# Kernel tuning notes

Measured on AMD Instinct MI355X. Metric: run time of the kernel, lower is better.

## Reference

```python
import jax, jax.numpy as jnp
import numpy as np
import math

N_HEADS = 4
GELU = lambda x: jax.nn.gelu(x, approximate=False)  # torch nn.GELU default = exact erf

def _ln(x, s, b):
    m = jnp.mean(x, axis=-1, keepdims=True)
    v = jnp.mean((x - m) ** 2, axis=-1, keepdims=True)
    return (x - m) * jax.lax.rsqrt(v + 1e-5) * s + b

def _fwd(materials, in_seq, proj_vars, param_vars, enc_w1, enc_b1, enc_w2, enc_b2, sos,
         tl_wq, tl_wk, tl_wv, tl_bq, tl_bk, tl_bv, tl_wo, tl_bo,
         tl_ln1s, tl_ln1b, tl_ln2s, tl_ln2b, tl_fw1, tl_fb1, tl_fw2, tl_fb2,
         pw1, pb1, pw2, pb2, pw3, pb3, pw4, pb4, pw5, pb5,
         ipw1, ipb1, ipw2, ipb2, hw1, hb1, hw2, hb2, hw3, hb3):
    B = in_seq.shape[0]
    # encoder input MLP: [B,S,1] -> [B,S,D]
    x = GELU(in_seq @ enc_w1 + enc_b1) @ enc_w2 + enc_b2
    x = jnp.concatenate([jnp.broadcast_to(sos, (B, 1, sos.shape[-1])), x], axis=1)
    S1, D = x.shape[1], x.shape[2]
    dh = D // N_HEADS
    # sinusoidal positional encoding
    pos = jnp.arange(S1, dtype=jnp.float32)[:, None]
    div = jnp.exp(jnp.arange(0, D, 2, dtype=jnp.float32) * (-math.log(10000.0) / D))
    ang = pos * div
    pe = jnp.stack([jnp.sin(ang), jnp.cos(ang)], axis=-1).reshape(S1, D)
    x = x + pe
    scale = 1.0 / math.sqrt(dh)
    # post-LN TransformerEncoder layers (torch default norm_first=False), eval mode (no dropout)
    for l in range(tl_wq.shape[0]):
        q = (x @ tl_wq[l] + tl_bq[l]).reshape(B, S1, N_HEADS, dh).transpose(0, 2, 1, 3)
        k = (x @ tl_wk[l] + tl_bk[l]).reshape(B, S1, N_HEADS, dh).transpose(0, 2, 1, 3)
        v = (x @ tl_wv[l] + tl_bv[l]).reshape(B, S1, N_HEADS, dh).transpose(0, 2, 1, 3)
        att = jax.nn.softmax(jnp.einsum('bhqd,bhkd->bhqk', q, k) * scale, axis=-1)
        o = jnp.einsum('bhqk,bhkd->bhqd', att, v).transpose(0, 2, 1, 3).reshape(B, S1, D)
        x = _ln(x + o @ tl_wo[l] + tl_bo[l], tl_ln1s[l], tl_ln1b[l])
        f = GELU(x @ tl_fw1[l] + tl_fb1[l]) @ tl_fw2[l] + tl_fb2[l]
        x = _ln(x + f, tl_ln2s[l], tl_ln2b[l])
    sos_out = x[:, 0]
    h = jnp.concatenate([proj_vars, sos_out], axis=1)
    for w, b in ((pw1, pb1), (pw2, pb2), (pw3, pb3), (pw4, pb4)):
        h = GELU(h @ w + b)
    proj_out = h @ pw5 + pb5
    pp = GELU(param_vars @ ipw1 + ipb1) @ ipw2 + ipb2
    mi = jnp.concatenate([pp, proj_out], axis=1)  # [B, output_features+param_vars]
    # MaterialHead mask-gather-MLP-scatter == run every tiny head densely, pick by material id
    h1 = GELU(jnp.einsum('bi,mio->mbo', mi, hw1) + hb1[:, None, :])
    h2 = GELU(jnp.einsum('mbi,mio->mbo', h1, hw2) + hb2[:, None, :])
    h3 = jnp.einsum('mbi,mio->mbo', h2, hw3) + hb3[:, None, :]  # [M,B,1]
    return h3[materials, jnp.arange(B)]  # [B,1]

def setup_inputs() -> dict:
    key = jax.random.key(0)
    ks = iter(jax.random.split(key, 64))
    def rn(shape, scale=0.05):
        return jax.random.normal(next(ks), shape, dtype=jnp.float32) * scale
    B, S, IN, EL, D, L, DFF = 64, 1024, 1, 48, 64, 3, 256
    PV, PP, OF, M = 3, 3, 24, 3
    IF = OF + PP
    return dict(
        in_seq=rn((B, S, IN), 1.0),
        proj_vars=rn((B, PV), 1.0),
        param_vars=rn((B, PP), 1.0),
        materials=jax.random.randint(next(ks), (B,), 0, M),
        enc_w1=rn((IN, EL)), enc_b1=rn((EL,)), enc_w2=rn((EL, D)), enc_b2=rn((D,)),
        sos=rn((1, 1, D)),
        tl_wq=rn((L, D, D)), tl_wk=rn((L, D, D)), tl_wv=rn((L, D, D)),
        tl_bq=rn((L, D)), tl_bk=rn((L, D)), tl_bv=rn((L, D)),
        tl_wo=rn((L, D, D)), tl_bo=rn((L, D)),
        tl_ln1s=jnp.ones((L, D)), tl_ln1b=jnp.zeros((L, D)),
        tl_ln2s=jnp.ones((L, D)), tl_ln2b=jnp.zeros((L, D)),
        tl_fw1=rn((L, D, DFF)), tl_fb1=rn((L, DFF)), tl_fw2=rn((L, DFF, D)), tl_fb2=rn((L, D)),
        pw1=rn((PV + D, 34)), pb1=rn((34,)), pw2=rn((34, 11)), pb2=rn((11,)),
        pw3=rn((11, 36)), pb3=rn((36,)), pw4=rn((36, 22)), pb4=rn((22,)),
        pw5=rn((22, OF)), pb5=rn((OF,)),
        ipw1=rn((PP, 3)), ipb1=rn((3,)), ipw2=rn((3, PP)), ipb2=rn((PP,)),
        hw1=rn((M, IF, 15)), hb1=rn((M, 15)), hw2=rn((M, 15, 18)), hb2=rn((M, 18)),
        hw3=rn((M, 18, 1)), hb3=rn((M, 1)),
    )

def reference(in_seq, proj_vars, param_vars, materials, enc_w1, enc_b1, enc_w2, enc_b2, sos,
              tl_wq, tl_wk, tl_wv, tl_bq, tl_bk, tl_bv, tl_wo, tl_bo,
              tl_ln1s, tl_ln1b, tl_ln2s, tl_ln2b, tl_fw1, tl_fb1, tl_fw2, tl_fb2,
              pw1, pb1, pw2, pb2, pw3, pb3, pw4, pb4, pw5, pb5,
              ipw1, ipb1, ipw2, ipb2, hw1, hb1, hw2, hb2, hw3, hb3):
    return _fwd(materials, in_seq, proj_vars, param_vars, enc_w1, enc_b1, enc_w2, enc_b2, sos,
                tl_wq, tl_wk, tl_wv, tl_bq, tl_bk, tl_bv, tl_wo, tl_bo,
                tl_ln1s, tl_ln1b, tl_ln2s, tl_ln2b, tl_fw1, tl_fb1, tl_fw2, tl_fb2,
                pw1, pb1, pw2, pb2, pw3, pb3, pw4, pb4, pw5, pb5,
                ipw1, ipb1, ipw2, ipb2, hw1, hb1, hw2, hb2, hw3, hb3)
```

## Files before the change

### kernel.cpp

```cpp
#include <hip/hip_runtime.h>
#include <hip/hip_bf16.h>
#include <math.h>

#define BB   64
#define SS   1024
#define S1C  1025
#define DD   64
#define NHD  4
#define NBH  (BB * NHD)
#define DHD  16
#define DFFC 256
#define NLAY 3
#define NTOK (BB * S1C)
#define SPAD 1056
#define TGRP2 9
#define FTT   16
#define HPAD 264
#define OPAD 68
#define YPAD 72
#define QSCL 0.36067376022224085f

typedef const float* fp;
typedef __attribute__((ext_vector_type(8))) short bf16x8;
typedef __attribute__((ext_vector_type(4))) float f32x4;

#if __has_builtin(__builtin_amdgcn_exp2f)
#define RAW_EXP2(x) __builtin_amdgcn_exp2f(x)
#else
#define RAW_EXP2(x) __expf(0.6931471805599453f * (x))
#endif
#if __has_builtin(__builtin_amdgcn_rcpf)
#define RAW_RCP(x) __builtin_amdgcn_rcpf(x)
#else
#define RAW_RCP(x) (1.0f / (x))
#endif

__device__ __forceinline__ float gelu_exact(float x) {
    return 0.5f * x * (1.0f + erff(x * 0.7071067811865475f));
}
__device__ __forceinline__ float erf_fast(float x) {
    float ax = fabsf(x);
    float t = RAW_RCP(1.0f + 0.3275911f * ax);
    float p = t * (0.254829592f + t * (-0.284496736f + t * (1.421413741f +
              t * (-1.453152027f + t * 1.061405429f))));
    float e = RAW_EXP2(ax * ax * -1.4426950408889634f);
    float r = 1.0f - p * e;
    return copysignf(r, x);
}
__device__ __forceinline__ float gelu_fast(float x) {
    return 0.5f * x * (1.0f + erf_fast(x * 0.7071067811865475f));
}
__device__ __forceinline__ short f2b(float f) {
    unsigned u = __float_as_uint(f);
    return (short)((u + 0x7fffu + ((u >> 16) & 1u)) >> 16);
}
__device__ __forceinline__ short f2b_pos(float f) {
    return (short)((__float_as_uint(f) + 0x8000u) >> 16);
}

__global__ __launch_bounds__(256) void k_wconv(
    fp wq, fp wk, fp wv, fp wo, fp w1, fp w2,
    short* __restrict__ wqkvT, short* __restrict__ woT,
    short* __restrict__ w1T, short* __restrict__ w2T)
{
    int l = blockIdx.y;
    int i = blockIdx.x * 256 + threadIdx.x;
    if (i < 12288) {
        int p = i >> 12, rem = i & 4095;
        int d = rem >> 6, j = rem & 63;
        fp src = (p == 0 ? wq : p == 1 ? wk : wv) + (size_t)l * 4096;
        float v = src[j * 64 + d];
        if (p == 0) v *= QSCL;
        wqkvT[(size_t)l * 12288 + i] = f2b(v);
    } else if (i < 16384) {
        int rem = i - 12288;
        woT[(size_t)l * 4096 + rem] = f2b(wo[(size_t)l * 4096 + (rem & 63) * 64 + (rem >> 6)]);
    } else if (i < 32768) {
        int rem = i - 16384;
        w1T[(size_t)l * 16384 + rem] = f2b(w1[(size_t)l * 16384 + (rem & 63) * 256 + (rem >> 6)]);
    } else {
        int rem = i - 32768;
        w2T[(size_t)l * 16384 + rem] = f2b(w2[(size_t)l * 16384 + (rem & 255) * 64 + (rem >> 8)]);
    }
}

__global__ __launch_bounds__(64) void k_zero(
    short* __restrict__ qb, short* __restrict__ kb, short* __restrict__ vbt)
{
    int bh = blockIdx.x, t = threadIdx.x;
    for (int i = t; i < 31 * 16; i += 64) {
        int r = i >> 4, c = i & 15;
        size_t idx = ((size_t)bh * SPAD + 1025 + r) * 16 + c;
        qb[idx] = 0; kb[idx] = 0;
    }
    for (int i = t; i < 16 * 31; i += 64) {
        int e = i / 31, c = i % 31;
        vbt[((size_t)bh * 16 + e) * SPAD + 1025 + c] = 0;
    }
}

__global__ __launch_bounds__(64) void k_encode(
    fp in_seq, fp enc_w1, fp enc_b1, fp enc_w2, fp enc_b2, fp sos,
    float* __restrict__ x, short* __restrict__ xb)
{
    int tok = blockIdx.x;
    int b = tok / S1C, s = tok % S1C;
    int d = threadIdx.x;
    __shared__ float e[48];
    float val;
    if (s == 0) {
        val = sos[d];
    } else {
        float t = in_seq[b * SS + (s - 1)];
        if (d < 48) e[d] = gelu_fast(t * enc_w1[d] + enc_b1[d]);
        __syncthreads();
        float acc = enc_b2[d];
        for (int j = 0; j < 48; ++j) acc += e[j] * enc_w2[j * DD + d];
        val = acc;
    }
    int i2 = (d >> 1) * 2;
    float factor = expf((float)i2 * (-9.210340371976184f / 64.0f));
    float ang = (float)s * factor;
    val += (d & 1) ? cosf(ang) : sinf(ang);
    x[(size_t)tok * DD + d] = val;
    xb[(size_t)tok * DD + d] = f2b(val);
}

__global__ __launch_bounds__(256) void k_qkv(
    const short* __restrict__ xb, const short* __restrict__ wqkvT,
    fp bq, fp bk, fp bv,
    short* __restrict__ qb, short* __restrict__ kb, short* __restrict__ vbt)
{
    int blk = blockIdx.x, t = threadIdx.x;
    int tok0 = blk * FTT;
    int w = t >> 6, l = t & 63;
    int quad = l >> 4, lo = l & 15;

    bf16x8 a0 = *(const bf16x8*)(xb + ((size_t)(tok0 + lo)) * DD + quad * 8);
    bf16x8 a1 = *(const bf16x8*)(xb + ((size_t)(tok0 + lo)) * DD + 32 + quad * 8);

    int tokr[4], br[4], sr[4];
    #pragma unroll
    for (int r = 0; r < 4; ++r) {
        tokr[r] = tok0 + quad * 4 + r;
        br[r] = tokr[r] / S1C; sr[r] = tokr[r] % S1C;
    }

    int n = w * 16 + lo;
    #pragma unroll
    for (int p = 0; p < 3; ++p) {
        const short* wT = wqkvT + (size_t)p * 4096 + (size_t)n * 64;
        bf16x8 b0 = *(const bf16x8*)(wT + quad * 8);
        bf16x8 b1 = *(const bf16x8*)(wT + 32 + quad * 8);
        f32x4 c = __builtin_amdgcn_mfma_f32_16x16x32_bf16(a0, b0, (f32x4){0,0,0,0}, 0, 0, 0);
        c = __builtin_amdgcn_mfma_f32_16x16x32_bf16(a1, b1, c, 0, 0, 0);
        float bias = (p == 0) ? bq[n] * QSCL : (p == 1) ? bk[n] : bv[n];
        #pragma unroll
        for (int r = 0; r < 4; ++r) {
            int bh = br[r] * NHD + w;
            short val = f2b(c[r] + bias);
            if (p == 0)      qb[((size_t)bh * SPAD + sr[r]) * 16 + lo] = val;
            else if (p == 1) kb[((size_t)bh * SPAD + sr[r]) * 16 + lo] = val;
            else             vbt[((size_t)bh * 16 + lo) * SPAD + sr[r]] = val;
        }
    }
}

__global__ __launch_bounds__(256) void k_attn(
    const short* __restrict__ qb, const short* __restrict__ kb,
    const short* __restrict__ vbt, short* __restrict__ ob)
{
    int bid = blockIdx.x;
    int bh  = bid % NBH;
    int grp = bid / NBH;
    int b = bh >> 2, h = bh & 3;
    int t = threadIdx.x;
    int w = t >> 6, l = t & 63;
    int quad = l >> 4, lo = l & 15;
    int t0 = grp * 4 + w;
    int t1 = t0 + 36;
    if (t1 > 65) t1 = 65;
    int qg0 = t0 * 16, qg1 = t1 * 16;

    __shared__ short pt_all[4][2][16][40];
    short (*pt0)[40] = pt_all[w][0];
    short (*pt1)[40] = pt_all[w][1];

    const short* qbase = qb + (size_t)bh * SPAD * 16;
    const short* kbase = kb + (size_t)bh * SPAD * 16;
    const short* vbase = vbt + (size_t)bh * 16 * SPAD;

    bf16x8 aQ0 = {0,0,0,0,0,0,0,0}, aQ1 = {0,0,0,0,0,0,0,0};
    if (quad < 2) {
        aQ0 = *(const bf16x8*)(qbase + ((size_t)(qg0 + lo)) * 16 + quad * 8);
        aQ1 = *(const bf16x8*)(qbase + ((size_t)(qg1 + lo)) * 16 + quad * 8);
    }

    const short ONE = 0x3F80;
    bf16x8 aOne = {ONE, ONE, ONE, ONE, ONE, ONE, ONE, ONE};

    f32x4 oc0 = {0.f,0.f,0.f,0.f}, oc1 = {0.f,0.f,0.f,0.f};
    f32x4 dn0 = {0.f,0.f,0.f,0.f}, dn1 = {0.f,0.f,0.f,0.f};

    for (int ch = 0; ch < 32; ++ch) {
        #pragma unroll
        for (int t01 = 0; t01 < 2; ++t01) {
            int krow = ch * 32 + t01 * 16 + lo;
            bf16x8 bK = *(const bf16x8*)(kbase + (size_t)krow * 16 + (quad & 1) * 8);
            f32x4 c0 = __builtin_amdgcn_mfma_f32_16x16x32_bf16(
                aQ0, bK, (f32x4){0.f,0.f,0.f,0.f}, 0, 0, 0);
            f32x4 c1 = __builtin_amdgcn_mfma_f32_16x16x32_bf16(
                aQ1, bK, (f32x4){0.f,0.f,0.f,0.f}, 0, 0, 0);
            #pragma unroll
            for (int r = 0; r < 4; ++r) {
                pt0[quad * 4 + r][t01 * 16 + lo] = f2b_pos(RAW_EXP2(c0[r]));
                pt1[quad * 4 + r][t01 * 16 + lo] = f2b_pos(RAW_EXP2(c1[r]));
            }
        }
        bf16x8 aV = *(const bf16x8*)(vbase + (size_t)lo * SPAD + ch * 32 + quad * 8);
        bf16x8 pB0 = *(const bf16x8*)&pt0[lo][quad * 8];
        oc0 = __builtin_amdgcn_mfma_f32_16x16x32_bf16(aV, pB0, oc0, 0, 0, 0);
        dn0 = __builtin_amdgcn_mfma_f32_16x16x32_bf16(aOne, pB0, dn0, 0, 0, 0);
        bf16x8 pB1 = *(const bf16x8*)&pt1[lo][quad * 8];
        oc1 = __builtin_amdgcn_mfma_f32_16x16x32_bf16(aV, pB1, oc1, 0, 0, 0);
        dn1 = __builtin_amdgcn_mfma_f32_16x16x32_bf16(aOne, pB1, dn1, 0, 0, 0);
    }
    {
        #pragma unroll
        for (int t01 = 0; t01 < 2; ++t01) {
            int krow = 1024 + t01 * 16 + lo;
            bf16x8 bK = *(const bf16x8*)(kbase + (size_t)krow * 16 + (quad & 1) * 8);
            f32x4 c0 = __builtin_amdgcn_mfma_f32_16x16x32_bf16(
                aQ0, bK, (f32x4){0.f,0.f,0.f,0.f}, 0, 0, 0);
            f32x4 c1 = __builtin_amdgcn_mfma_f32_16x16x32_bf16(
                aQ1, bK, (f32x4){0.f,0.f,0.f,0.f}, 0, 0, 0);
            bool valid = (krow <= 1024);
            #pragma unroll
            for (int r = 0; r < 4; ++r) {
                pt0[quad * 4 + r][t01 * 16 + lo] = f2b_pos(valid ? RAW_EXP2(c0[r]) : 0.f);
                pt1[quad * 4 + r][t01 * 16 + lo] = f2b_pos(valid ? RAW_EXP2(c1[r]) : 0.f);
            }
        }
        bf16x8 aV = *(const bf16x8*)(vbase + (size_t)lo * SPAD + 1024 + quad * 8);
        bf16x8 pB0 = *(const bf16x8*)&pt0[lo][quad * 8];
        oc0 = __builtin_amdgcn_mfma_f32_16x16x32_bf16(aV, pB0, oc0, 0, 0, 0);
        dn0 = __builtin_amdgcn_mfma_f32_16x16x32_bf16(aOne, pB0, dn0, 0, 0, 0);
        bf16x8 pB1 = *(const bf16x8*)&pt1[lo][quad * 8];
        oc1 = __builtin_amdgcn_mfma_f32_16x16x32_bf16(aV, pB1, oc1, 0, 0, 0);
        dn1 = __builtin_amdgcn_mfma_f32_16x16x32_bf16(aOne, pB1, dn1, 0, 0, 0);
    }

    {
        int qrow = qg0 + lo;
        if (qrow < S1C) {
            float inv = 1.0f / dn0[0];
            unsigned p0 = (unsigned short)f2b(oc0[0] * inv) | ((unsigned)(unsigned short)f2b(oc0[1] * inv) << 16);
            unsigned p1 = (unsigned short)f2b(oc0[2] * inv) | ((unsigned)(unsigned short)f2b(oc0[3] * inv) << 16);
            *(uint2*)(ob + ((size_t)b * S1C + qrow) * DD + h * DHD + quad * 4) = make_uint2(p0, p1);
        }
    }
    {
        int qrow = qg1 + lo;
        if (qrow < S1C) {
            float inv = 1.0f / dn1[0];
            unsigned p0 = (unsigned short)f2b(oc1[0] * inv) | ((unsigned)(unsigned short)f2b(oc1[1] * inv) << 16);
            unsigned p1 = (unsigned short)f2b(oc1[2] * inv) | ((unsigned)(unsigned short)f2b(oc1[3] * inv) << 16);
            *(uint2*)(ob + ((size_t)b * S1C + qrow) * DD + h * DHD + quad * 4) = make_uint2(p0, p1);
        }
    }
}

__global__ __launch_bounds__(256) void k_block(
    const short* __restrict__ ob, float* __restrict__ x,
    const short* __restrict__ woT, fp bo, fp ln1s, fp ln1b,
    const short* __restrict__ w1T, fp b1, const short* __restrict__ w2T, fp b2,
    fp ln2s, fp ln2b,
    const short* __restrict__ wqkvTn, fp bqn, fp bkn, fp bvn,
    short* __restrict__ qb, short* __restrict__ kb, short* __restrict__ vbt,
    int has_next)
{
    int blk = blockIdx.x, t = threadIdx.x;
    int tok0 = blk * FTT;
    int w = t >> 6, l = t & 63;
    int quad = l >> 4, lo = l & 15;

    __shared__ float otf[FTT][OPAD];
    __shared__ short ys[FTT][YPAD];
    __shared__ short hid[FTT][HPAD];

    {
        bf16x8 a0 = *(const bf16x8*)(ob + ((size_t)(tok0 + lo)) * DD + quad * 8);
        bf16x8 a1 = *(const bf16x8*)(ob + ((size_t)(tok0 + lo)) * DD + 32 + quad * 8);
        int n = w * 16 + lo;
        const short* wT = woT + (size_t)n * 64;
        bf16x8 b0 = *(const bf16x8*)(wT + quad * 8);
        bf16x8 bb = *(const bf16x8*)(wT + 32 + quad * 8);
        f32x4 c = __builtin_amdgcn_mfma_f32_16x16x32_bf16(a0, b0, (f32x4){0,0,0,0}, 0, 0, 0);
        c = __builtin_amdgcn_mfma_f32_16x16x32_bf16(a1, bb, c, 0, 0, 0);
        float bov = bo[n];
        #pragma unroll
        for (int r = 0; r < 4; ++r) otf[quad * 4 + r][n] = c[r] + bov;
    }
    __syncthreads();

    int d = l;
    float yv[4];
    {
        float s1 = ln1s[d], bl1 = ln1b[d];
        #pragma unroll
        for (int i = 0; i < 4; ++i) {
            int tt = w * 4 + i;
            float val = otf[tt][d] + x[(size_t)(tok0 + tt) * DD + d];
            float sum = val;
            for (int off = 32; off > 0; off >>= 1) sum += __shfl_xor(sum, off, 64);
            float mean = sum * (1.0f / 64.0f);
            float c = val - mean;
            float vs = c * c;
            for (int off = 32; off > 0; off >>= 1) vs += __shfl_xor(vs, off, 64);
            float y = c / sqrtf(vs * (1.0f / 64.0f) + 1e-5f) * s1 + bl1;
            yv[i] = y;
            ys[tt][d] = f2b(y);
        }
    }
    __syncthreads();

    {
        bf16x8 a0 = *(const bf16x8*)&ys[lo][quad * 8];
        bf16x8 a1 = *(const bf16x8*)&ys[lo][32 + quad * 8];
        #pragma unroll
        for (int i = 0; i < 4; ++i) {
            int n = w * 64 + i * 16 + lo;
            const short* wT = w1T + (size_t)n * 64;
            bf16x8 b0 = *(const bf16x8*)(wT + quad * 8);
            bf16x8 bb = *(const bf16x8*)(wT + 32 + quad * 8);
            f32x4 c = __builtin_amdgcn_mfma_f32_16x16x32_bf16(a0, b0, (f32x4){0,0,0,0}, 0, 0, 0);
            c = __builtin_amdgcn_mfma_f32_16x16x32_bf16(a1, bb, c, 0, 0, 0);
            float b1v = b1[n];
            #pragma unroll
            for (int r = 0; r < 4; ++r)
                hid[quad * 4 + r][n] = f2b(gelu_fast(c[r] + b1v));
        }
    }
    __syncthreads();

    {
        f32x4 c2 = {0.f, 0.f, 0.f, 0.f};
        const short* wT2 = w2T + (size_t)(w * 16 + lo) * 256;
        #pragma unroll
        for (int kc = 0; kc < 8; ++kc) {
            bf16x8 a2 = *(const bf16x8*)&hid[lo][kc * 32 + quad * 8];
            bf16x8 b2f = *(const bf16x8*)(wT2 + kc * 32 + quad * 8);
            c2 = __builtin_amdgcn_mfma_f32_16x16x32_bf16(a2, b2f, c2, 0, 0, 0);
        }
        float b2v = b2[w * 16 + lo];
        #pragma unroll
        for (int r = 0; r < 4; ++r)
            otf[quad * 4 + r][w * 16 + lo] = c2[r] + b2v;
    }
    __syncthreads();

    {
        float s2 = ln2s[d], bl2 = ln2b[d];
        #pragma unroll
        for (int i = 0; i < 4; ++i) {
            int tt = w * 4 + i;
            float val = otf[tt][d] + yv[i];
            float sum = val;
            for (int off = 32; off > 0; off >>= 1) sum += __shfl_xor(sum, off, 64);
            float mean = sum * (1.0f / 64.0f);
            float c = val - mean;
            float vs = c * c;
            for (int off = 32; off > 0; off >>= 1) vs += __shfl_xor(vs, off, 64);
            float y = c / sqrtf(vs * (1.0f / 64.0f) + 1e-5f) * s2 + bl2;
            x[(size_t)(tok0 + tt) * DD + d] = y;
            ys[tt][d] = f2b(y);
        }
    }
    __syncthreads();

    if (has_next) {
        bf16x8 a0 = *(const bf16x8*)&ys[lo][quad * 8];
        bf16x8 a1 = *(const bf16x8*)&ys[lo][32 + quad * 8];
        int tokr[4], br[4], sr[4];
        #pragma unroll
        for (int r = 0; r < 4; ++r) {
            tokr[r] = tok0 + quad * 4 + r;
            br[r] = tokr[r] / S1C; sr[r] = tokr[r] % S1C;
        }
        int n = w * 16 + lo;
        #pragma unroll
        for (int p = 0; p < 3; ++p) {
            const short* wT = wqkvTn + (size_t)p * 4096 + (size_t)n * 64;
            bf16x8 b0 = *(const bf16x8*)(wT + quad * 8);
            bf16x8 bb = *(const bf16x8*)(wT + 32 + quad * 8);
            f32x4 c = __builtin_amdgcn_mfma_f32_16x16x32_bf16(a0, b0, (f32x4){0,0,0,0}, 0, 0, 0);
            c = __builtin_amdgcn_mfma_f32_16x16x32_bf16(a1, bb, c, 0, 0, 0);
            float bias = (p == 0) ? bqn[n] * QSCL : (p == 1) ? bkn[n] : bvn[n];
            #pragma unroll
            for (int r = 0; r < 4; ++r) {
                int bh = br[r] * NHD + w;
                short val = f2b(c[r] + bias);
                if (p == 0)      qb[((size_t)bh * SPAD + sr[r]) * 16 + lo] = val;
                else if (p == 1) kb[((size_t)bh * SPAD + sr[r]) * 16 + lo] = val;
                else             vbt[((size_t)bh * 16 + lo) * SPAD + sr[r]] = val;
            }
        }
    }
}

__global__ __launch_bounds__(64) void k_head(
    const float* __restrict__ x, fp proj_vars, fp param_vars,
    const int* __restrict__ materials,
    fp pw1, fp pb1, fp pw2, fp pb2, fp pw3, fp pb3,
    fp pw4, fp pb4, fp pw5, fp pb5,
    fp ipw1, fp ipb1, fp ipw2, fp ipb2,
    fp hw1, fp hb1, fp hw2, fp hb2, fp hw3, fp hb3,
    float* __restrict__ out)
{
    int b = blockIdx.x;
    int tid = threadIdx.x;
    __shared__ float A[80], Bf[80], pp[8], mi[32];

    if (tid < 3) A[tid] = proj_vars[b * 3 + tid];
    A[3 + tid] = x[((size_t)b * S1C + 0) * DD + tid];
    __syncthreads();

    if (tid < 34) {
        float a = pb1[tid];
        for (int i = 0; i < 67; ++i) a += A[i] * pw1[i * 34 + tid];
        Bf[tid] = gelu_exact(a);
    }
    __syncthreads();
    if (tid < 11) {
        float a = pb2[tid];
        for (int i = 0; i < 34; ++i) a += Bf[i] * pw2[i * 11 + tid];
        A[tid] = gelu_exact(a);
    }
    __syncthreads();
    if (tid < 36) {
        float a = pb3[tid];
        for (int i = 0; i < 11; ++i) a += A[i] * pw3[i * 36 + tid];
        Bf[tid] = gelu_exact(a);
    }
    __syncthreads();
    if (tid < 22) {
        float a = pb4[tid];
        for (int i = 0; i < 36; ++i) a += Bf[i] * pw4[i * 22 + tid];
        A[tid] = gelu_exact(a);
    }
    __syncthreads();
    if (tid < 24) {
        float a = pb5[tid];
        for (int i = 0; i < 22; ++i) a += A[i] * pw5[i * 24 + tid];
        mi[3 + tid] = a;
    }
    if (tid < 3) {
        float a = ipb1[tid];
        for (int i = 0; i < 3; ++i) a += param_vars[b * 3 + i] * ipw1[i * 3 + tid];
        pp[tid] = gelu_exact(a);
    }
    __syncthreads();
    if (tid < 3) {
        float a = ipb2[tid];
        for (int i = 0; i < 3; ++i) a += pp[i] * ipw2[i * 3 + tid];
        mi[tid] = a;
    }
    __syncthreads();

    int m = materials[b];
    if (tid < 15) {
        float a = hb1[m * 15 + tid];
        for (int i = 0; i < 27; ++i) a += mi[i] * hw1[(m * 27 + i) * 15 + tid];
        A[tid] = gelu_exact(a);
    }
    __syncthreads();
    if (tid < 18) {
        float a = hb2[m * 18 + tid];
        for (int i = 0; i < 15; ++i) a += A[i] * hw2[(m * 15 + i) * 18 + tid];
        Bf[tid] = gelu_exact(a);
    }
    __syncthreads();
    if (tid == 0) {
        float a = hb3[m];
        for (int i = 0; i < 18; ++i) a += Bf[i] * hw3[m * 18 + i];
        out[b] = a;
    }
}

extern "C" void kernel_launch(void* const* d_in, const int* in_sizes, int n_in,
                              void* d_out, int out_size, void* d_ws, size_t ws_size,
                              hipStream_t stream) {
    fp in_seq     = (fp)d_in[0];
    fp proj_vars  = (fp)d_in[1];
    fp param_vars = (fp)d_in[2];
    const int* materials = (const int*)d_in[3];
    fp enc_w1 = (fp)d_in[4];
    fp enc_b1 = (fp)d_in[5];
    fp enc_w2 = (fp)d_in[6];
    fp enc_b2 = (fp)d_in[7];
    fp sos    = (fp)d_in[8];
    fp tl_wq  = (fp)d_in[9];
    fp tl_wk  = (fp)d_in[10];
    fp tl_wv  = (fp)d_in[11];
    fp tl_bq  = (fp)d_in[12];
    fp tl_bk  = (fp)d_in[13];
    fp tl_bv  = (fp)d_in[14];
    fp tl_wo  = (fp)d_in[15];
    fp tl_bo  = (fp)d_in[16];
    fp tl_ln1s = (fp)d_in[17];
    fp tl_ln1b = (fp)d_in[18];
    fp tl_ln2s = (fp)d_in[19];
    fp tl_ln2b = (fp)d_in[20];
    fp tl_fw1 = (fp)d_in[21];
    fp tl_fb1 = (fp)d_in[22];
    fp tl_fw2 = (fp)d_in[23];
    fp tl_fb2 = (fp)d_in[24];
    fp pw1 = (fp)d_in[25]; fp pb1 = (fp)d_in[26];
    fp pw2 = (fp)d_in[27]; fp pb2 = (fp)d_in[28];
    fp pw3 = (fp)d_in[29]; fp pb3 = (fp)d_in[30];
    fp pw4 = (fp)d_in[31]; fp pb4 = (fp)d_in[32];
    fp pw5 = (fp)d_in[33]; fp pb5 = (fp)d_in[34];
    fp ipw1 = (fp)d_in[35]; fp ipb1 = (fp)d_in[36];
    fp ipw2 = (fp)d_in[37]; fp ipb2 = (fp)d_in[38];
    fp hw1 = (fp)d_in[39]; fp hb1 = (fp)d_in[40];
    fp hw2 = (fp)d_in[41]; fp hb2 = (fp)d_in[42];
    fp hw3 = (fp)d_in[43]; fp hb3 = (fp)d_in[44];

    float* x  = (float*)d_ws;
    short* ob = (short*)(x + (size_t)NTOK * DD);
    short* xb = ob + (size_t)NTOK * DD;
    short* qb = xb + (size_t)NTOK * DD;
    short* kb = qb + (size_t)NBH * SPAD * 16;
    short* vbt = kb + (size_t)NBH * SPAD * 16;
    short* wqkvT = vbt + (size_t)NBH * 16 * SPAD;
    short* woT = wqkvT + (size_t)NLAY * 12288;
    short* w1T = woT + (size_t)NLAY * 4096;
    short* w2T = w1T + (size_t)NLAY * 16384;

    k_wconv<<<dim3(192, NLAY), 256, 0, stream>>>(
        tl_wq, tl_wk, tl_wv, tl_wo, tl_fw1, tl_fw2, wqkvT, woT, w1T, w2T);
    k_zero<<<NBH, 64, 0, stream>>>(qb, kb, vbt);
    k_encode<<<NTOK, 64, 0, stream>>>(in_seq, enc_w1, enc_b1, enc_w2, enc_b2, sos, x, xb);

    k_qkv<<<NTOK / FTT, 256, 0, stream>>>(
        xb, wqkvT,
        tl_bq, tl_bk, tl_bv,
        qb, kb, vbt);

    for (int l = 0; l < NLAY; ++l) {
        k_attn<<<NBH * TGRP2, 256, 0, stream>>>(qb, kb, vbt, ob);
        int ln = (l + 1 < NLAY) ? (l + 1) : l;
        k_block<<<NTOK / FTT, 256, 0, stream>>>(
            ob, x,
            woT + (size_t)l * 4096, tl_bo + (size_t)l * DD,
            tl_ln1s + (size_t)l * DD, tl_ln1b + (size_t)l * DD,
            w1T + (size_t)l * 16384, tl_fb1 + (size_t)l * DFFC,
            w2T + (size_t)l * 16384, tl_fb2 + (size_t)l * DD,
            tl_ln2s + (size_t)l * DD, tl_ln2b + (size_t)l * DD,
            wqkvT + (size_t)ln * 12288,
            tl_bq + (size_t)ln * DD, tl_bk + (size_t)ln * DD, tl_bv + (size_t)ln * DD,
            qb, kb, vbt,
            (l + 1 < NLAY) ? 1 : 0);
    }

    k_head<<<BB, 64, 0, stream>>>(
        x, proj_vars, param_vars, materials,
        pw1, pb1, pw2, pb2, pw3, pb3, pw4, pb4, pw5, pb5,
        ipw1, ipb1, ipw2, ipb2,
        hw1, hb1, hw2, hb2, hw3, hb3,
        (float*)d_out);
}
```

Before: 555.4 us.

## Process 32 tokens per k_block and batch 4 tokens per encode block

```diff
diff --git a/kernel.cpp b/kernel.cpp
--- a/kernel.cpp
+++ b/kernel.cpp
@@ -15,6 +15,7 @@
 #define SPAD 1056
 #define TGRP2 9
 #define FTT   16
+#define FT2   32
 #define HPAD 264
 #define OPAD 68
 #define YPAD 72
@@ -99,29 +100,29 @@
     }
 }
 
-__global__ __launch_bounds__(64) void k_encode(
+__global__ __launch_bounds__(256) void k_encode(
     fp in_seq, fp enc_w1, fp enc_b1, fp enc_w2, fp enc_b2, fp sos,
     float* __restrict__ x, short* __restrict__ xb)
 {
-    int tok = blockIdx.x;
+    int t = threadIdx.x;
+    int w = t >> 6, d = t & 63;
+    int tok = blockIdx.x * 4 + w;
     int b = tok / S1C, s = tok % S1C;
-    int d = threadIdx.x;
-    __shared__ float e[48];
+    __shared__ float e[4][48];
     float val;
     if (s == 0) {
         val = sos[d];
     } else {
-        float t = in_seq[b * SS + (s - 1)];
-        if (d < 48) e[d] = gelu_fast(t * enc_w1[d] + enc_b1[d]);
-        __syncthreads();
+        float tin = in_seq[b * SS + (s - 1)];
+        if (d < 48) e[w][d] = gelu_fast(tin * enc_w1[d] + enc_b1[d]);
         float acc = enc_b2[d];
-        for (int j = 0; j < 48; ++j) acc += e[j] * enc_w2[j * DD + d];
+        for (int j = 0; j < 48; ++j) acc += e[w][j] * enc_w2[j * DD + d];
         val = acc;
     }
     int i2 = (d >> 1) * 2;
-    float factor = expf((float)i2 * (-9.210340371976184f / 64.0f));
+    float factor = RAW_EXP2((float)i2 * (-9.210340371976184f / 64.0f) * 1.4426950408889634f);
     float ang = (float)s * factor;
-    val += (d & 1) ? cosf(ang) : sinf(ang);
+    val += (d & 1) ? __cosf(ang) : __sinf(ang);
     x[(size_t)tok * DD + d] = val;
     xb[(size_t)tok * DD + d] = f2b(val);
 }
@@ -280,44 +281,55 @@
     int has_next)
 {
     int blk = blockIdx.x, t = threadIdx.x;
-    int tok0 = blk * FTT;
+    int tok0 = blk * FT2;
     int w = t >> 6, l = t & 63;
     int quad = l >> 4, lo = l & 15;
 
-    __shared__ float otf[FTT][OPAD];
-    __shared__ short ys[FTT][YPAD];
-    __shared__ short hid[FTT][HPAD];
-
-    {
-        bf16x8 a0 = *(const bf16x8*)(ob + ((size_t)(tok0 + lo)) * DD + quad * 8);
-        bf16x8 a1 = *(const bf16x8*)(ob + ((size_t)(tok0 + lo)) * DD + 32 + quad * 8);
+    __shared__ float otf[FT2][OPAD];
+    __shared__ short ys[FT2][YPAD];
+    __shared__ short hid[FT2][HPAD];
+
+    {
+        const short* obp0 = ob + ((size_t)(tok0 + lo)) * DD;
+        const short* obp1 = ob + ((size_t)(tok0 + 16 + lo)) * DD;
+        bf16x8 a0 = *(const bf16x8*)(obp0 + quad * 8);
+        bf16x8 a1 = *(const bf16x8*)(obp0 + 32 + quad * 8);
+        bf16x8 a2 = *(const bf16x8*)(obp1 + quad * 8);
+        bf16x8 a3 = *(const bf16x8*)(obp1 + 32 + quad * 8);
         int n = w * 16 + lo;
         const short* wT = woT + (size_t)n * 64;
         bf16x8 b0 = *(const bf16x8*)(wT + quad * 8);
         bf16x8 bb = *(const bf16x8*)(wT + 32 + quad * 8);
-        f32x4 c = __builtin_amdgcn_mfma_f32_16x16x32_bf16(a0, b0, (f32x4){0,0,0,0}, 0, 0, 0);
-        c = __builtin_amdgcn_mfma_f32_16x16x32_bf16(a1, bb, c, 0, 0, 0);
+        f32x4 c0 = __builtin_amdgcn_mfma_f32_16x16x32_bf16(a0, b0, (f32x4){0,0,0,0}, 0, 0, 0);
+        c0 = __builtin_amdgcn_mfma_f32_16x16x32_bf16(a1, bb, c0, 0, 0, 0);
+        f32x4 c1 = __builtin_amdgcn_mfma_f32_16x16x32_bf16(a2, b0, (f32x4){0,0,0,0}, 0, 0, 0);
+        c1 = __builtin_amdgcn_mfma_f32_16x16x32_bf16(a3, bb, c1, 0, 0, 0);
         float bov = bo[n];
         #pragma unroll
-        for (int r = 0; r < 4; ++r) otf[quad * 4 + r][n] = c[r] + bov;
+        for (int r = 0; r < 4; ++r) {
+            otf[quad * 4 + r][n] = c0[r] + bov;
+            otf[16 + quad * 4 + r][n] = c1[r] + bov;
+        }
     }
     __syncthreads();
 
     int d = l;
-    float yv[4];
+    float yv[8];
     {
         float s1 = ln1s[d], bl1 = ln1b[d];
         #pragma unroll
-        for (int i = 0; i < 4; ++i) {
-            int tt = w * 4 + i;
+        for (int i = 0; i < 8; ++i) {
+            int tt = w * 8 + i;
             float val = otf[tt][d] + x[(size_t)(tok0 + tt) * DD + d];
-            float sum = val;
-            for (int off = 32; off > 0; off >>= 1) sum += __shfl_xor(sum, off, 64);
+            float sum = val, vs = val * val;
+            #pragma unroll
+            for (int off = 32; off > 0; off >>= 1) {
+                sum += __shfl_xor(sum, off, 64);
+                vs  += __shfl_xor(vs, off, 64);
+            }
             float mean = sum * (1.0f / 64.0f);
-            float c = val - mean;
-            float vs = c * c;
-            for (int off = 32; off > 0; off >>= 1) vs += __shfl_xor(vs, off, 64);
-            float y = c / sqrtf(vs * (1.0f / 64.0f) + 1e-5f) * s1 + bl1;
+            float var = vs * (1.0f / 64.0f) - mean * mean;
+            float y = (val - mean) * rsqrtf(var + 1e-5f) * s1 + bl1;
             yv[i] = y;
             ys[tt][d] = f2b(y);
         }
@@ -327,51 +339,63 @@
     {
         bf16x8 a0 = *(const bf16x8*)&ys[lo][quad * 8];
         bf16x8 a1 = *(const bf16x8*)&ys[lo][32 + quad * 8];
+        bf16x8 a2 = *(const bf16x8*)&ys[16 + lo][quad * 8];
+        bf16x8 a3 = *(const bf16x8*)&ys[16 + lo][32 + quad * 8];
         #pragma unroll
         for (int i = 0; i < 4; ++i) {
             int n = w * 64 + i * 16 + lo;
             const short* wT = w1T + (size_t)n * 64;
             bf16x8 b0 = *(const bf16x8*)(wT + quad * 8);
             bf16x8 bb = *(const bf16x8*)(wT + 32 + quad * 8);
-            f32x4 c = __builtin_amdgcn_mfma_f32_16x16x32_bf16(a0, b0, (f32x4){0,0,0,0}, 0, 0, 0);
-            c = __builtin_amdgcn_mfma_f32_16x16x32_bf16(a1, bb, c, 0, 0, 0);
+            f32x4 c0 = __builtin_amdgcn_mfma_f32_16x16x32_bf16(a0, b0, (f32x4){0,0,0,0}, 0, 0, 0);
+            c0 = __builtin_amdgcn_mfma_f32_16x16x32_bf16(a1, bb, c0, 0, 0, 0);
+            f32x4 c1 = __builtin_amdgcn_mfma_f32_16x16x32_bf16(a2, b0, (f32x4){0,0,0,0}, 0, 0, 0);
+            c1 = __builtin_amdgcn_mfma_f32_16x16x32_bf16(a3, bb, c1, 0, 0, 0);
             float b1v = b1[n];
             #pragma unroll
-            for (int r = 0; r < 4; ++r)
-                hid[quad * 4 + r][n] = f2b(gelu_fast(c[r] + b1v));
-        }
-    }
-    __syncthreads();
-
-    {
-        f32x4 c2 = {0.f, 0.f, 0.f, 0.f};
+            for (int r = 0; r < 4; ++r) {
+                hid[quad * 4 + r][n] = f2b(gelu_fast(c0[r] + b1v));
+                hid[16 + quad * 4 + r][n] = f2b(gelu_fast(c1[r] + b1v));
+            }
+        }
+    }
+    __syncthreads();
+
+    {
+        f32x4 c20 = {0.f,0.f,0.f,0.f}, c21 = {0.f,0.f,0.f,0.f};
         const short* wT2 = w2T + (size_t)(w * 16 + lo) * 256;
         #pragma unroll
         for (int kc = 0; kc < 8; ++kc) {
-            bf16x8 a2 = *(const bf16x8*)&hid[lo][kc * 32 + quad * 8];
             bf16x8 b2f = *(const bf16x8*)(wT2 + kc * 32 + quad * 8);
-            c2 = __builtin_amdgcn_mfma_f32_16x16x32_bf16(a2, b2f, c2, 0, 0, 0);
+            bf16x8 a20 = *(const bf16x8*)&hid[lo][kc * 32 + quad * 8];
+            bf16x8 a21 = *(const bf16x8*)&hid[16 + lo][kc * 32 + quad * 8];
+            c20 = __builtin_amdgcn_mfma_f32_16x16x32_bf16(a20, b2f, c20, 0, 0, 0);
+            c21 = __builtin_amdgcn_mfma_f32_16x16x32_bf16(a21, b2f, c21, 0, 0, 0);
         }
         float b2v = b2[w * 16 + lo];
         #pragma unroll
-        for (int r = 0; r < 4; ++r)
-            otf[quad * 4 + r][w * 16 + lo] = c2[r] + b2v;
+        for (int r = 0; r < 4; ++r) {
+            otf[quad * 4 + r][w * 16 + lo] = c20[r] + b2v;
+            otf[16 + quad * 4 + r][w * 16 + lo] = c21[r] + b2v;
+        }
     }
     __syncthreads();
 
     {
         float s2 = ln2s[d], bl2 = ln2b[d];
         #pragma unroll
-        for (int i = 0; i < 4; ++i) {
-            int tt = w * 4 + i;
+        for (int i = 0; i < 8; ++i) {
+            int tt = w * 8 + i;
             float val = otf[tt][d] + yv[i];
-            float sum = val;
-            for (int off = 32; off > 0; off >>= 1) sum += __shfl_xor(sum, off, 64);
+            float sum = val, vs = val * val;
+            #pragma unroll
+            for (int off = 32; off > 0; off >>= 1) {
+                sum += __shfl_xor(sum, off, 64);
+                vs  += __shfl_xor(vs, off, 64);
+            }
             float mean = sum * (1.0f / 64.0f);
-            float c = val - mean;
-            float vs = c * c;
-            for (int off = 32; off > 0; off >>= 1) vs += __shfl_xor(vs, off, 64);
-            float y = c / sqrtf(vs * (1.0f / 64.0f) + 1e-5f) * s2 + bl2;
+            float var = vs * (1.0f / 64.0f) - mean * mean;
+            float y = (val - mean) * rsqrtf(var + 1e-5f) * s2 + bl2;
             x[(size_t)(tok0 + tt) * DD + d] = y;
             ys[tt][d] = f2b(y);
         }
@@ -381,28 +405,39 @@
     if (has_next) {
         bf16x8 a0 = *(const bf16x8*)&ys[lo][quad * 8];
         bf16x8 a1 = *(const bf16x8*)&ys[lo][32 + quad * 8];
-        int tokr[4], br[4], sr[4];
-        #pragma unroll
-        for (int r = 0; r < 4; ++r) {
-            tokr[r] = tok0 + quad * 4 + r;
-            br[r] = tokr[r] / S1C; sr[r] = tokr[r] % S1C;
-        }
+        bf16x8 a2 = *(const bf16x8*)&ys[16 + lo][quad * 8];
+        bf16x8 a3 = *(const bf16x8*)&ys[16 + lo][32 + quad * 8];
         int n = w * 16 + lo;
         #pragma unroll
         for (int p = 0; p < 3; ++p) {
             const short* wT = wqkvTn + (size_t)p * 4096 + (size_t)n * 64;
             bf16x8 b0 = *(const bf16x8*)(wT + quad * 8);
             bf16x8 bb = *(const bf16x8*)(wT + 32 + quad * 8);
-            f32x4 c = __builtin_amdgcn_mfma_f32_16x16x32_bf16(a0, b0, (f32x4){0,0,0,0}, 0, 0, 0);
-            c = __builtin_amdgcn_mfma_f32_16x16x32_bf16(a1, bb, c, 0, 0, 0);
+            f32x4 c0 = __builtin_amdgcn_mfma_f32_16x16x32_bf16(a0, b0, (f32x4){0,0,0,0}, 0, 0, 0);
+            c0 = __builtin_amdgcn_mfma_f32_16x16x32_bf16(a1, bb, c0, 0, 0, 0);
+            f32x4 c1 = __builtin_amdgcn_mfma_f32_16x16x32_bf16(a2, b0, (f32x4){0,0,0,0}, 0, 0, 0);
+            c1 = __builtin_amdgcn_mfma_f32_16x16x32_bf16(a3, bb, c1, 0, 0, 0);
             float bias = (p == 0) ? bqn[n] * QSCL : (p == 1) ? bkn[n] : bvn[n];
             #pragma unroll
             for (int r = 0; r < 4; ++r) {
-                int bh = br[r] * NHD + w;
-                short val = f2b(c[r] + bias);
-                if (p == 0)      qb[((size_t)bh * SPAD + sr[r]) * 16 + lo] = val;
-                else if (p == 1) kb[((size_t)bh * SPAD + sr[r]) * 16 + lo] = val;
-                else             vbt[((size_t)bh * 16 + lo) * SPAD + sr[r]] = val;
+                int tok = tok0 + quad * 4 + r;
+                int bb0 = tok / S1C, ss0 = tok % S1C;
+                int bh = bb0 * NHD + w;
+                short val = f2b(c0[r] + bias);
+                int tok2 = tok + 16;
+                int bb1 = tok2 / S1C, ss1 = tok2 % S1C;
+                int bh2 = bb1 * NHD + w;
+                short val2 = f2b(c1[r] + bias);
+                if (p == 0) {
+                    qb[((size_t)bh * SPAD + ss0) * 16 + lo] = val;
+                    qb[((size_t)bh2 * SPAD + ss1) * 16 + lo] = val2;
+                } else if (p == 1) {
+                    kb[((size_t)bh * SPAD + ss0) * 16 + lo] = val;
+                    kb[((size_t)bh2 * SPAD + ss1) * 16 + lo] = val2;
+                } else {
+                    vbt[((size_t)bh * 16 + lo) * SPAD + ss0] = val;
+                    vbt[((size_t)bh2 * 16 + lo) * SPAD + ss1] = val2;
+                }
             }
         }
     }
@@ -540,7 +575,7 @@
     k_wconv<<<dim3(192, NLAY), 256, 0, stream>>>(
         tl_wq, tl_wk, tl_wv, tl_wo, tl_fw1, tl_fw2, wqkvT, woT, w1T, w2T);
     k_zero<<<NBH, 64, 0, stream>>>(qb, kb, vbt);
-    k_encode<<<NTOK, 64, 0, stream>>>(in_seq, enc_w1, enc_b1, enc_w2, enc_b2, sos, x, xb);
+    k_encode<<<NTOK / 4, 256, 0, stream>>>(in_seq, enc_w1, enc_b1, enc_w2, enc_b2, sos, x, xb);
 
     k_qkv<<<NTOK / FTT, 256, 0, stream>>>(
         xb, wqkvT,
@@ -550,7 +585,7 @@
     for (int l = 0; l < NLAY; ++l) {
         k_attn<<<NBH * TGRP2, 256, 0, stream>>>(qb, kb, vbt, ob);
         int ln = (l + 1 < NLAY) ? (l + 1) : l;
-        k_block<<<NTOK / FTT, 256, 0, stream>>>(
+        k_block<<<NTOK / FT2, 256, 0, stream>>>(
             ob, x,
             woT + (size_t)l * 4096, tl_bo + (size_t)l * DD,
             tl_ln1s + (size_t)l * DD, tl_ln1b + (size_t)l * DD,
```

Result: faster. 530.0 us (-4.6%).
